# Kernel tuning notes

Measured on AMD Instinct MI355X. Metric: run time of the kernel, lower is better.

## Reference

```python
import jax, jax.numpy as jnp
import numpy as np

EPS = 1e-5  # torch F.layer_norm default

def _layer_norm(x):
    mu = jnp.mean(x, axis=-1, keepdims=True)
    var = jnp.mean((x - mu) ** 2, axis=-1, keepdims=True)
    return (x - mu) * jax.lax.rsqrt(var + EPS)

def setup_inputs() -> dict:
    key = jax.random.key(0)
    k1, k2, k3, k4 = jax.random.split(key, 4)
    B, T, d, n = 4, 32, 256, 1024
    return {
        "x_seq": jax.random.normal(k1, (B, T, d), jnp.float32),
        "targets": jax.random.normal(k2, (B, T, d), jnp.float32),
        "E": jax.random.normal(k3, (d, n), jnp.float32) * 0.1,
        "Dy": jax.random.normal(k4, (n, d), jnp.float32) * 0.1,
    }

def reference(x_seq, targets, E, Dy):
    B, T, d = x_seq.shape
    n = E.shape[1]
    # Precompute per-step neuron activations (no cross-step dependency here)
    x_neurons = jax.nn.relu(_layer_norm(x_seq @ E))      # [B,T,n]
    tgt_neurons = jax.nn.relu(_layer_norm(targets @ E))  # [B,T,n]
    # update at step t uses targets[:, t+1]; last step does no update
    tgt_next = jnp.concatenate(
        [tgt_neurons[:, 1:], jnp.zeros_like(tgt_neurons[:, :1])], axis=1)
    upd_mask = jnp.arange(T) < (T - 1)  # [T]

    G0 = jnp.tile(0.01 * jnp.eye(n, dtype=x_seq.dtype)[None], (B, 1, 1))

    def step(G, inp):
        xn, tn, m = inp  # [B,n], [B,n], scalar bool
        p1 = jnp.einsum('bn,bnm->bm', xn, G)
        p2 = jnp.einsum('bn,bnm->bm', p1, G)
        p3 = jnp.einsum('bn,bnm->bm', p2, G)
        reasoning = jnp.maximum(p1, jnp.maximum(p2, p3))
        y = jax.nn.relu(reasoning @ Dy)  # [B,d]
        # rank-1 Hebbian max-update: G = max(G, 0.5 * xn tn^T)
        upd = 0.5 * xn[:, :, None] * tn[:, None, :]
        G_new = jnp.where(m, jnp.maximum(G, upd), G)
        return G_new, y

    xs = (jnp.swapaxes(x_neurons, 0, 1),  # [T,B,n]
          jnp.swapaxes(tgt_next, 0, 1),   # [T,B,n]
          upd_mask)                       # [T]
    _, ys = jax.lax.scan(step, G0, xs)    # ys: [T,B,d]
    return jnp.swapaxes(ys, 0, 1)         # [B,T,d]
```

## Files before the change

kernel.cpp:

```cpp
#include <hip/hip_runtime.h>

#define BB 4
#define TT 32
#define DD 256
#define NN 1024

#define XN_OFF   0
#define TN_OFF   131072
#define PB_OFF   262144
#define RB_OFF   524288
#define FLG_OFF  655360
#define FLG_WORDS 6144
#define WS_END   (FLG_OFF + FLG_WORDS)

__global__ __launch_bounds__(256) void precompute_kernel(
    const float* __restrict__ x_seq, const float* __restrict__ targets,
    const float* __restrict__ E, float* __restrict__ ws)
{
    __shared__ float xr[4][DD];
    __shared__ float redS[4][4], redSS[4][4];
    const int blk = blockIdx.x;
    const int bt0 = blk * 2, bt1 = bt0 + 1;
    const int tid = threadIdx.x;
    const int lane = tid & 63, w = tid >> 6;

    xr[0][tid] = x_seq[(size_t)bt0 * DD + tid];
    xr[1][tid] = x_seq[(size_t)bt1 * DD + tid];
    xr[2][tid] = targets[(size_t)bt0 * DD + tid];
    xr[3][tid] = targets[(size_t)bt1 * DD + tid];
    __syncthreads();

    const float4* E4 = (const float4*)E;
    float4 acc[4];
#pragma unroll
    for (int r = 0; r < 4; ++r) acc[r] = make_float4(0.f, 0.f, 0.f, 0.f);
#pragma unroll 4
    for (int k = 0; k < DD; ++k) {
        float4 e = E4[(size_t)k * (NN / 4) + tid];
#pragma unroll
        for (int r = 0; r < 4; ++r) {
            float xv = xr[r][k];
            acc[r].x += xv * e.x; acc[r].y += xv * e.y;
            acc[r].z += xv * e.z; acc[r].w += xv * e.w;
        }
    }
    float s[4], ss[4];
#pragma unroll
    for (int r = 0; r < 4; ++r) {
        s[r]  = acc[r].x + acc[r].y + acc[r].z + acc[r].w;
        ss[r] = acc[r].x*acc[r].x + acc[r].y*acc[r].y + acc[r].z*acc[r].z + acc[r].w*acc[r].w;
    }
#pragma unroll
    for (int d = 1; d < 64; d <<= 1) {
#pragma unroll
        for (int r = 0; r < 4; ++r) {
            s[r]  += __shfl_xor(s[r], d, 64);
            ss[r] += __shfl_xor(ss[r], d, 64);
        }
    }
    if (lane == 0) {
#pragma unroll
        for (int r = 0; r < 4; ++r) { redS[w][r] = s[r]; redSS[w][r] = ss[r]; }
    }
    __syncthreads();
#pragma unroll
    for (int r = 0; r < 4; ++r) {
        s[r]  = redS[0][r] + redS[1][r] + redS[2][r] + redS[3][r];
        ss[r] = redSS[0][r] + redSS[1][r] + redSS[2][r] + redSS[3][r];
    }
#pragma unroll
    for (int r = 0; r < 4; ++r) {
        const float mu  = s[r] * (1.0f / NN);
        const float var = ss[r] * (1.0f / NN) - mu * mu;
        const float inv = rsqrtf(var + 1e-5f);
        float4 o;
        o.x = fmaxf(0.f, (acc[r].x - mu) * inv);
        o.y = fmaxf(0.f, (acc[r].y - mu) * inv);
        o.z = fmaxf(0.f, (acc[r].z - mu) * inv);
        o.w = fmaxf(0.f, (acc[r].w - mu) * inv);
        const int bt = (r & 1) ? bt1 : bt0;
        float* dst = nullptr;
        if (r < 2) dst = ws + XN_OFF + (size_t)bt * NN;
        else if ((bt & 31) > 0) dst = ws + TN_OFF + (size_t)(bt - 1) * NN;
        if (dst) ((float4*)dst)[tid] = o;
    }
}

__device__ __forceinline__ float ald(const float* p) {
    return __hip_atomic_load(p, __ATOMIC_RELAXED, __HIP_MEMORY_SCOPE_AGENT);
}
__device__ __forceinline__ unsigned long long ald64(const unsigned long long* p) {
    return __hip_atomic_load(p, __ATOMIC_RELAXED, __HIP_MEMORY_SCOPE_AGENT);
}
__device__ __forceinline__ void ast(float* p, float v) {
    __hip_atomic_store(p, v, __ATOMIC_RELAXED, __HIP_MEMORY_SCOPE_AGENT);
}
__device__ __forceinline__ unsigned aldu_rlx(const unsigned* p) {
    return __hip_atomic_load(p, __ATOMIC_RELAXED, __HIP_MEMORY_SCOPE_AGENT);
}

__global__ __launch_bounds__(512, 1) void mega_kernel(
    const float* __restrict__ Dy, float* __restrict__ out, float* __restrict__ ws)
{
    __shared__ float sh[6144];
    const int blk = blockIdx.x;
    const int tid = threadIdx.x;

    float* pb     = ws + PB_OFF;
    float* rb     = ws + RB_OFF;
    unsigned* flg = (unsigned*)(ws + FLG_OFF);

    if (blk < 192) {
        const int stage = blk >> 6;
        const int b     = (blk >> 4) & 3;
        const int wg    = blk & 15;
        const int lane  = tid & 63;
        const int w     = tid >> 6;
        const int colbase = wg * 64 + w * 8;
        const int row0    = lane * 16;
        const float* xn = ws + XN_OFF + (size_t)b * TT * NN;
        const float* tn = ws + TN_OFF + (size_t)b * TT * NN;
        unsigned* myflag = flg + ((size_t)(stage * 4 + b) * 16 + wg) * 32;
        const unsigned* inflags =
            (stage > 0) ? flg + ((size_t)((stage - 1) * 4 + b) * 16) * 32 : (const unsigned*)0;
        unsigned seen = 0;

        float G[16][8];
#pragma unroll
        for (int i = 0; i < 16; ++i)
#pragma unroll
            for (int c = 0; c < 8; ++c)
                G[i][c] = (row0 + i == colbase + c) ? 0.01f : 0.0f;

#pragma unroll 1
        for (int t = 0; t < TT; t += 4) {
            const int bt = b * TT + t;
            float* pbase = pb + (size_t)bt * 2 * NN;

            float v1a = 0.f, v1b = 0.f, v1c = 0.f, v1d = 0.f;

            if (stage != 0) {
                const unsigned tgt = (unsigned)(t + 4);
                if (tid < 64) {
                    if (seen < tgt) {
                        const unsigned* p = inflags + (size_t)(tid & 15) * 32;
                        int g = 0;
                        for (;;) {
                            unsigned v = aldu_rlx(p);
                            if (v > seen) seen = v;
                            if (__all(seen >= tgt)) break;
                            __builtin_amdgcn_s_sleep(1);
                            if (++g > (1 << 22)) break;
                        }
                    }
                }
                __syncthreads();
                asm volatile("" ::: "memory");
                if (stage == 2) {
                    const int co8 = colbase + (lane & 7);
                    v1a = ald(pbase + (size_t)0 * NN + co8);
                    v1b = ald(pbase + (size_t)2 * NN + co8);
                    v1c = ald(pbase + (size_t)4 * NN + co8);
                    v1d = ald(pbase + (size_t)6 * NN + co8);
                }
                const size_t soff = (stage == 1) ? 0 : NN;
                const unsigned long long* s0 =
                    (const unsigned long long*)(pbase + (size_t)0 * NN + soff);
                const unsigned long long* s1 =
                    (const unsigned long long*)(pbase + (size_t)2 * NN + soff);
                const unsigned long long* s2 =
                    (const unsigned long long*)(pbase + (size_t)4 * NN + soff);
                const unsigned long long* s3 =
                    (const unsigned long long*)(pbase + (size_t)6 * NN + soff);
                const unsigned long long g0 = ald64(s0 + tid);
                const unsigned long long g1 = ald64(s1 + tid);
                const unsigned long long g2 = ald64(s2 + tid);
                const unsigned long long g3 = ald64(s3 + tid);
                const int e0 = 2 * tid;
                const int eo = e0 + (e0 >> 4);
                sh[0 * 1152 + eo]     = __uint_as_float((unsigned)g0);
                sh[0 * 1152 + eo + 1] = __uint_as_float((unsigned)(g0 >> 32));
                sh[1 * 1152 + eo]     = __uint_as_float((unsigned)g1);
                sh[1 * 1152 + eo + 1] = __uint_as_float((unsigned)(g1 >> 32));
                sh[2 * 1152 + eo]     = __uint_as_float((unsigned)g2);
                sh[2 * 1152 + eo + 1] = __uint_as_float((unsigned)(g2 >> 32));
                sh[3 * 1152 + eo]     = __uint_as_float((unsigned)g3);
                sh[3 * 1152 + eo + 1] = __uint_as_float((unsigned)(g3 >> 32));
                __syncthreads();
            }

#pragma unroll
            for (int j = 0; j < 4; ++j) {
                const int tj = t + j;
                float in[16];
                if (stage == 0) {
                    const float4* xp = (const float4*)(xn + (size_t)tj * NN + row0);
                    float4 q0 = xp[0], q1 = xp[1], q2 = xp[2], q3 = xp[3];
                    in[0]=q0.x; in[1]=q0.y; in[2]=q0.z; in[3]=q0.w;
                    in[4]=q1.x; in[5]=q1.y; in[6]=q1.z; in[7]=q1.w;
                    in[8]=q2.x; in[9]=q2.y; in[10]=q2.z; in[11]=q2.w;
                    in[12]=q3.x; in[13]=q3.y; in[14]=q3.z; in[15]=q3.w;
                } else {
#pragma unroll
                    for (int k = 0; k < 16; ++k) in[k] = sh[j * 1152 + lane * 17 + k];
                }

                float acc[8] = {0.f,0.f,0.f,0.f,0.f,0.f,0.f,0.f};
#pragma unroll
                for (int i = 0; i < 16; ++i)
#pragma unroll
                    for (int c = 0; c < 8; ++c) acc[c] += in[i] * G[i][c];

                float t4[8];
#pragma unroll
                for (int c = 0; c < 8; ++c) t4[c] = __shfl_xor(acc[c], 4, 64);
                const bool k2 = (lane & 4) != 0;
                float s4[4];
#pragma unroll
                for (int k = 0; k < 4; ++k) s4[k] = k2 ? (acc[4+k] + t4[4+k]) : (acc[k] + t4[k]);
                float t2[4];
#pragma unroll
                for (int k = 0; k < 4; ++k) t2[k] = __shfl_xor(s4[k], 2, 64);
                const bool k1 = (lane & 2) != 0;
                float s2[2];
#pragma unroll
                for (int k = 0; k < 2; ++k) s2[k] = k1 ? (s4[2+k] + t2[2+k]) : (s4[k] + t2[k]);
                float t1[2];
#pragma unroll
                for (int k = 0; k < 2; ++k) t1[k] = __shfl_xor(s2[k], 1, 64);
                float v = (lane & 1) ? (s2[1] + t1[1]) : (s2[0] + t1[0]);
                v += __shfl_xor(v, 8, 64);
                v += __shfl_xor(v, 16, 64);
                v += __shfl_xor(v, 32, 64);

                if (stage == 0) {
                    if (lane < 8) ast(pbase + (size_t)(2 * j) * NN + colbase + lane, v);
                } else if (stage == 1) {
                    if (lane < 8) ast(pbase + (size_t)(2 * j) * NN + NN + colbase + lane, v);
                } else {
                    const int c = colbase + (lane & 7);
                    const float v2own = sh[j * 1152 + c + (c >> 4)];
                    const float v1o = (j == 0) ? v1a : (j == 1) ? v1b : (j == 2) ? v1c : v1d;
                    float r = fmaxf(v, fmaxf(v1o, v2own));
                    if (lane < 8) ast(rb + (size_t)(bt + j) * NN + colbase + lane, r);
                }

                if (j < 3) {
                    float x[16];
                    if (stage == 0) {
#pragma unroll
                        for (int k = 0; k < 16; ++k) x[k] = in[k];
                    } else {
                        const float4* xp = (const float4*)(xn + (size_t)tj * NN + row0);
                        float4 q0 = xp[0], q1 = xp[1], q2 = xp[2], q3 = xp[3];
                        x[0]=q0.x; x[1]=q0.y; x[2]=q0.z; x[3]=q0.w;
                        x[4]=q1.x; x[5]=q1.y; x[6]=q1.z; x[7]=q1.w;
                        x[8]=q2.x; x[9]=q2.y; x[10]=q2.z; x[11]=q2.w;
                        x[12]=q3.x; x[13]=q3.y; x[14]=q3.z; x[15]=q3.w;
                    }
                    const float4 ta = *(const float4*)(tn + (size_t)tj * NN + colbase);
                    const float4 tb = *(const float4*)(tn + (size_t)tj * NN + colbase + 4);
                    const float tv[8] = {0.5f*ta.x, 0.5f*ta.y, 0.5f*ta.z, 0.5f*ta.w,
                                         0.5f*tb.x, 0.5f*tb.y, 0.5f*tb.z, 0.5f*tb.w};
#pragma unroll
                    for (int c = 0; c < 8; ++c)
#pragma unroll
                        for (int i = 0; i < 16; ++i)
                            G[i][c] = fmaxf(G[i][c], x[i] * tv[c]);
                }
            }

            __syncthreads();
            if (tid == 0)
                __hip_atomic_store(myflag, (unsigned)(t + 4),
                                   __ATOMIC_RELEASE, __HIP_MEMORY_SCOPE_AGENT);

            if (t + 3 < TT - 1) {
                const int tj = t + 3;
                const float4* xp = (const float4*)(xn + (size_t)tj * NN + row0);
                float4 q0 = xp[0], q1 = xp[1], q2 = xp[2], q3 = xp[3];
                float x[16];
                x[0]=q0.x; x[1]=q0.y; x[2]=q0.z; x[3]=q0.w;
                x[4]=q1.x; x[5]=q1.y; x[6]=q1.z; x[7]=q1.w;
                x[8]=q2.x; x[9]=q2.y; x[10]=q2.z; x[11]=q2.w;
                x[12]=q3.x; x[13]=q3.y; x[14]=q3.z; x[15]=q3.w;
                const float4 ta = *(const float4*)(tn + (size_t)tj * NN + colbase);
                const float4 tb = *(const float4*)(tn + (size_t)tj * NN + colbase + 4);
                const float tv[8] = {0.5f*ta.x, 0.5f*ta.y, 0.5f*ta.z, 0.5f*ta.w,
                                     0.5f*tb.x, 0.5f*tb.y, 0.5f*tb.z, 0.5f*tb.w};
#pragma unroll
                for (int c = 0; c < 8; ++c)
#pragma unroll
                    for (int i = 0; i < 16; ++i)
                        G[i][c] = fmaxf(G[i][c], x[i] * tv[c]);
            }
        }
    } else {
        const int k   = blk - 192;
        const int b   = k >> 3;
        const int t0  = (k & 7) * 4;
        const int bt0 = b * TT + t0;
        if (tid < 64) {
            const unsigned* p = flg + ((size_t)(2 * 4 + b) * 16 + (tid & 15)) * 32;
            const unsigned tgt = (unsigned)(t0 + 4);
            int g = 0;
            for (;;) {
                unsigned v = aldu_rlx(p);
                if (__all(v >= tgt)) break;
                __builtin_amdgcn_s_sleep(1);
                if (++g > (1 << 22)) break;
            }
        }
        __syncthreads();
        asm volatile("" ::: "memory");
#pragma unroll
        for (int j = 0; j < 4; ++j) {
            const float* r = rb + (size_t)(bt0 + j) * NN;
            sh[tid * 4 + j]         = ald(r + tid);
            sh[(tid + 512) * 4 + j] = ald(r + tid + 512);
        }
        __syncthreads();
        const int d = tid & 255, h = tid >> 8;
        float acc[4] = {0.f, 0.f, 0.f, 0.f};
        const int n0 = h * 512;
#pragma unroll 8
        for (int n = n0; n < n0 + 512; ++n) {
            const float dv = Dy[(size_t)n * DD + d];
            const float4 rv = *(const float4*)&sh[n * 4];
            acc[0] += rv.x * dv; acc[1] += rv.y * dv;
            acc[2] += rv.z * dv; acc[3] += rv.w * dv;
        }
#pragma unroll
        for (int j = 0; j < 4; ++j) sh[4096 + (h * 4 + j) * 256 + d] = acc[j];
        __syncthreads();
        if (tid < 256) {
#pragma unroll
            for (int j = 0; j < 4; ++j)
                out[(size_t)(bt0 + j) * DD + tid] =
                    fmaxf(0.f, sh[4096 + j * 256 + tid] + sh[4096 + (4 + j) * 256 + tid]);
        }
    }
}

extern "C" void kernel_launch(void* const* d_in, const int* in_sizes, int n_in,
                              void* d_out, int out_size, void* d_ws, size_t ws_size,
                              hipStream_t stream) {
    const float* x_seq   = (const float*)d_in[0];
    const float* targets = (const float*)d_in[1];
    const float* E       = (const float*)d_in[2];
    const float* Dy      = (const float*)d_in[3];
    float* out = (float*)d_out;
    float* ws  = (float*)d_ws;

    hipMemsetAsync(ws + FLG_OFF, 0, (size_t)FLG_WORDS * sizeof(unsigned), stream);

    precompute_kernel<<<BB * TT / 2, 256, 0, stream>>>(x_seq, targets, E, ws);
    mega_kernel<<<224, 512, 0, stream>>>(Dy, out, ws);
}
```

Measured before the change: 204.0 us.

## Split pipeline stages across twice as many 256-thread blocks

Halves the block size of the persistent pipelined kernel from 512 to 256 threads and doubles the number of blocks. Each recurrence-stage block now owns 32 columns instead of 64, the flag array grows to match, and the output-projection blocks each handle 2 timesteps instead of 4. The goal is to spread the serial recurrence over more compute units (448 blocks instead of 224) so each block does less work per step. In exchange, every stage has to wait on twice as many producer flags. All 448 blocks must also be resident at once, or the spin-waits could deadlock.

```diff
diff --git a/kernel.cpp b/kernel.cpp
--- a/kernel.cpp
+++ b/kernel.cpp
@@ -10,7 +10,7 @@
 #define PB_OFF   262144
 #define RB_OFF   524288
 #define FLG_OFF  655360
-#define FLG_WORDS 6144
+#define FLG_WORDS 12288
 #define WS_END   (FLG_OFF + FLG_WORDS)
 
 __global__ __launch_bounds__(256) void precompute_kernel(
@@ -99,10 +99,10 @@
     return __hip_atomic_load(p, __ATOMIC_RELAXED, __HIP_MEMORY_SCOPE_AGENT);
 }
 
-__global__ __launch_bounds__(512, 1) void mega_kernel(
+__global__ __launch_bounds__(256, 2) void mega_kernel(
     const float* __restrict__ Dy, float* __restrict__ out, float* __restrict__ ws)
 {
-    __shared__ float sh[6144];
+    __shared__ float sh[4608];
     const int blk = blockIdx.x;
     const int tid = threadIdx.x;
 
@@ -110,19 +110,19 @@
     float* rb     = ws + RB_OFF;
     unsigned* flg = (unsigned*)(ws + FLG_OFF);
 
-    if (blk < 192) {
-        const int stage = blk >> 6;
-        const int b     = (blk >> 4) & 3;
-        const int wg    = blk & 15;
+    if (blk < 384) {
+        const int stage = blk >> 7;
+        const int b     = (blk >> 5) & 3;
+        const int wg    = blk & 31;
         const int lane  = tid & 63;
         const int w     = tid >> 6;
-        const int colbase = wg * 64 + w * 8;
+        const int colbase = wg * 32 + w * 8;
         const int row0    = lane * 16;
         const float* xn = ws + XN_OFF + (size_t)b * TT * NN;
         const float* tn = ws + TN_OFF + (size_t)b * TT * NN;
-        unsigned* myflag = flg + ((size_t)(stage * 4 + b) * 16 + wg) * 32;
+        unsigned* myflag = flg + ((size_t)((stage * 4 + b) * 32 + wg)) * 32;
         const unsigned* inflags =
-            (stage > 0) ? flg + ((size_t)((stage - 1) * 4 + b) * 16) * 32 : (const unsigned*)0;
+            (stage > 0) ? flg + ((size_t)((stage - 1) * 4 + b) * 32) * 32 : (const unsigned*)0;
         unsigned seen = 0;
 
         float G[16][8];
@@ -143,7 +143,7 @@
                 const unsigned tgt = (unsigned)(t + 4);
                 if (tid < 64) {
                     if (seen < tgt) {
-                        const unsigned* p = inflags + (size_t)(tid & 15) * 32;
+                        const unsigned* p = inflags + (size_t)(tid & 31) * 32;
                         int g = 0;
                         for (;;) {
                             unsigned v = aldu_rlx(p);
@@ -172,20 +172,29 @@
                     (const unsigned long long*)(pbase + (size_t)4 * NN + soff);
                 const unsigned long long* s3 =
                     (const unsigned long long*)(pbase + (size_t)6 * NN + soff);
-                const unsigned long long g0 = ald64(s0 + tid);
-                const unsigned long long g1 = ald64(s1 + tid);
-                const unsigned long long g2 = ald64(s2 + tid);
-                const unsigned long long g3 = ald64(s3 + tid);
-                const int e0 = 2 * tid;
+                const int u0 = 2 * tid, u1 = 2 * tid + 1;
+                const unsigned long long ga0 = ald64(s0 + u0), ga1 = ald64(s0 + u1);
+                const unsigned long long gb0 = ald64(s1 + u0), gb1 = ald64(s1 + u1);
+                const unsigned long long gc0 = ald64(s2 + u0), gc1 = ald64(s2 + u1);
+                const unsigned long long gd0 = ald64(s3 + u0), gd1 = ald64(s3 + u1);
+                const int e0 = 4 * tid;
                 const int eo = e0 + (e0 >> 4);
-                sh[0 * 1152 + eo]     = __uint_as_float((unsigned)g0);
-                sh[0 * 1152 + eo + 1] = __uint_as_float((unsigned)(g0 >> 32));
-                sh[1 * 1152 + eo]     = __uint_as_float((unsigned)g1);
-                sh[1 * 1152 + eo + 1] = __uint_as_float((unsigned)(g1 >> 32));
-                sh[2 * 1152 + eo]     = __uint_as_float((unsigned)g2);
-                sh[2 * 1152 + eo + 1] = __uint_as_float((unsigned)(g2 >> 32));
-                sh[3 * 1152 + eo]     = __uint_as_float((unsigned)g3);
-                sh[3 * 1152 + eo + 1] = __uint_as_float((unsigned)(g3 >> 32));
+                sh[0 * 1152 + eo]     = __uint_as_float((unsigned)ga0);
+                sh[0 * 1152 + eo + 1] = __uint_as_float((unsigned)(ga0 >> 32));
+                sh[0 * 1152 + eo + 2] = __uint_as_float((unsigned)ga1);
+                sh[0 * 1152 + eo + 3] = __uint_as_float((unsigned)(ga1 >> 32));
+                sh[1 * 1152 + eo]     = __uint_as_float((unsigned)gb0);
+                sh[1 * 1152 + eo + 1] = __uint_as_float((unsigned)(gb0 >> 32));
+                sh[1 * 1152 + eo + 2] = __uint_as_float((unsigned)gb1);
+                sh[1 * 1152 + eo + 3] = __uint_as_float((unsigned)(gb1 >> 32));
+                sh[2 * 1152 + eo]     = __uint_as_float((unsigned)gc0);
+                sh[2 * 1152 + eo + 1] = __uint_as_float((unsigned)(gc0 >> 32));
+                sh[2 * 1152 + eo + 2] = __uint_as_float((unsigned)gc1);
+                sh[2 * 1152 + eo + 3] = __uint_as_float((unsigned)(gc1 >> 32));
+                sh[3 * 1152 + eo]     = __uint_as_float((unsigned)gd0);
+                sh[3 * 1152 + eo + 1] = __uint_as_float((unsigned)(gd0 >> 32));
+                sh[3 * 1152 + eo + 2] = __uint_as_float((unsigned)gd1);
+                sh[3 * 1152 + eo + 3] = __uint_as_float((unsigned)(gd1 >> 32));
                 __syncthreads();
             }
 
@@ -296,13 +305,13 @@
             }
         }
     } else {
-        const int k   = blk - 192;
-        const int b   = k >> 3;
-        const int t0  = (k & 7) * 4;
+        const int k   = blk - 384;
+        const int b   = k >> 4;
+        const int t0  = (k & 15) * 2;
         const int bt0 = b * TT + t0;
         if (tid < 64) {
-            const unsigned* p = flg + ((size_t)(2 * 4 + b) * 16 + (tid & 15)) * 32;
-            const unsigned tgt = (unsigned)(t0 + 4);
+            const unsigned* p = flg + ((size_t)((2 * 4 + b) * 32 + (tid & 31))) * 32;
+            const unsigned tgt = (unsigned)(t0 + 2);
             int g = 0;
             for (;;) {
                 unsigned v = aldu_rlx(p);
@@ -314,31 +323,23 @@
         __syncthreads();
         asm volatile("" ::: "memory");
 #pragma unroll
-        for (int j = 0; j < 4; ++j) {
+        for (int j = 0; j < 2; ++j) {
             const float* r = rb + (size_t)(bt0 + j) * NN;
-            sh[tid * 4 + j]         = ald(r + tid);
-            sh[(tid + 512) * 4 + j] = ald(r + tid + 512);
+#pragma unroll
+            for (int kk = 0; kk < 4; ++kk)
+                sh[j * 1024 + tid + 256 * kk] = ald(r + tid + 256 * kk);
         }
         __syncthreads();
-        const int d = tid & 255, h = tid >> 8;
-        float acc[4] = {0.f, 0.f, 0.f, 0.f};
-        const int n0 = h * 512;
+        const int d = tid;
+        float acc0 = 0.f, acc1 = 0.f;
 #pragma unroll 8
-        for (int n = n0; n < n0 + 512; ++n) {
+        for (int n = 0; n < NN; ++n) {
             const float dv = Dy[(size_t)n * DD + d];
-            const float4 rv = *(const float4*)&sh[n * 4];
-            acc[0] += rv.x * dv; acc[1] += rv.y * dv;
-            acc[2] += rv.z * dv; acc[3] += rv.w * dv;
-        }
-#pragma unroll
-        for (int j = 0; j < 4; ++j) sh[4096 + (h * 4 + j) * 256 + d] = acc[j];
-        __syncthreads();
-        if (tid < 256) {
-#pragma unroll
-            for (int j = 0; j < 4; ++j)
-                out[(size_t)(bt0 + j) * DD + tid] =
-                    fmaxf(0.f, sh[4096 + j * 256 + tid] + sh[4096 + (4 + j) * 256 + tid]);
-        }
+            acc0 += sh[n] * dv;
+            acc1 += sh[1024 + n] * dv;
+        }
+        out[(size_t)bt0 * DD + d]       = fmaxf(0.f, acc0);
+        out[(size_t)(bt0 + 1) * DD + d] = fmaxf(0.f, acc1);
     }
 }
 
@@ -355,5 +356,5 @@
     hipMemsetAsync(ws + FLG_OFF, 0, (size_t)FLG_WORDS * sizeof(unsigned), stream);
 
     precompute_kernel<<<BB * TT / 2, 256, 0, stream>>>(x_seq, targets, E, ws);
-    mega_kernel<<<224, 512, 0, stream>>>(Dy, out, ws);
-}
+    mega_kernel<<<448, 256, 0, stream>>>(Dy, out, ws);
+}
```

Result: slower. 214.1 us (+4.9%).
